# Optimization experiments

Measured on AMD Instinct MI355X. Metric: run time of the kernel, lower is better.

Reference implementation:

```python
import jax, jax.numpy as jnp
import numpy as np
from jax import lax

BIG = jnp.float32(1e6)  # sentinel 1D distance for rows with no edge pixel


def _maxpool3(x):
    # torch MaxPool2d(kernel_size=3, stride=1, padding=1) on NCHW; pad value -inf
    return lax.reduce_window(x, -jnp.inf, lax.max,
                             window_dimensions=(1, 1, 3, 3),
                             window_strides=(1, 1, 1, 1),
                             padding='SAME')


def _gen_edge(bool_map):
    # eroded = bool_map AND bool(maxpool((~bool_map).float()))
    pooled = _maxpool3(jnp.logical_not(bool_map).astype(jnp.float32))
    return jnp.logical_and(bool_map, pooled > 0).astype(jnp.int32)


def _dist1d(edge):
    # 1D distance along last axis (W) to nearest edge==1 pixel. edge: [B,1,H,W] int
    e = jnp.moveaxis(edge, -1, 0)  # [W,B,1,H]
    init = jnp.full(e.shape[1:], BIG, dtype=jnp.float32)

    def step(carry, ei):
        d = jnp.where(ei > 0, jnp.float32(0.0), carry + 1.0)
        return d, d

    _, dfwd = lax.scan(step, init, e)
    _, dbwd = lax.scan(step, init, e[::-1])
    g = jnp.minimum(dfwd, dbwd[::-1])          # [W,B,1,H]
    return jnp.minimum(jnp.moveaxis(g, 0, -1), BIG)  # [B,1,H,W]


def _edt(edge):
    # Exact Euclidean distance transform to nearest edge==1 pixel (separable,
    # Felzenszwalb-Huttenlocher formulation: d^2(y,x) = min_y' (y-y')^2 + g(y',x)^2).
    g = _dist1d(edge)          # [B,1,H,W]
    g2 = (g * g)[:, 0]         # [B,H,W]
    H = edge.shape[2]
    y = jnp.arange(H, dtype=jnp.float32)
    ydiff2 = (y[:, None] - y[None, :]) ** 2   # [H, H'] squared row offsets

    def per_img(g2img):  # g2img: [H,W] -> [H,W]
        return jnp.min(ydiff2[:, :, None] + g2img[None, :, :], axis=1)

    d2 = lax.map(per_img, g2)  # sequential over batch to bound the [H,H,W] temp
    return jnp.sqrt(d2)[:, None]  # [B,1,H,W]


def setup_inputs() -> dict:
    key = jax.random.key(0)
    kp, kt = jax.random.split(key)
    B, C, H, W = 16, 1, 256, 256
    pred = jax.random.uniform(kp, (B, C, H, W), dtype=jnp.float32)
    target = jax.random.uniform(kt, (B, C, H, W), dtype=jnp.float32)
    return {"pred": pred, "target": target}


def reference(pred, target):
    pred_b = pred > 0.5
    target_b = target > 0.5
    pred_edge = _gen_edge(pred_b)      # [B,1,H,W] int32 in {0,1}
    target_edge = _gen_edge(target_b)  # [B,1,H,W] int32 in {0,1}
    # scipy: distance_transform_edt(1-edge) * (1-edge) => dist to nearest edge, 0 on edge
    target_dist = _edt(target_edge) * (1 - target_edge).astype(jnp.float32)
    multiplied = pred_edge.astype(jnp.float32) * target_dist
    return jnp.mean(multiplied)
```

## Files before the change

kernel.cpp:

```cpp
#include <hip/hip_runtime.h>
#include <math.h>

#define H 256
#define W 256
#define BATCH 16
#define XT 16

__device__ __constant__ float kBIG = 1.0e6f;

__global__ __launch_bounds__(256) void k_rowdist(const float* __restrict__ target,
                                                 float* __restrict__ g2out) {
    const int y = blockIdx.x;
    const int b = blockIdx.y;
    const int x = threadIdx.x;
    const float* timg = target + (size_t)b * H * W;

    __shared__ int   nt[3][W + 2];
    __shared__ float A[W], Bv[W];

    if (x < 3) { nt[x][0] = 0; nt[x][W + 1] = 0; }
    nt[0][x + 1] = (y > 0)     ? ((timg[(y - 1) * W + x] > 0.5f) ? 0 : 1) : 0;
    nt[1][x + 1] =               ((timg[ y      * W + x] > 0.5f) ? 0 : 1);
    nt[2][x + 1] = (y < H - 1) ? ((timg[(y + 1) * W + x] > 0.5f) ? 0 : 1) : 0;
    __syncthreads();

    int holes = 0;
    #pragma unroll
    for (int r = 0; r < 3; ++r)
        holes |= nt[r][x] | nt[r][x + 1] | nt[r][x + 2];
    const int edge = (nt[1][x + 1] == 0) && holes;

    const float f = edge ? 0.0f : 1.0e6f;
    A[x]  = f - (float)x;
    Bv[x] = f + (float)x;
    __syncthreads();

    #pragma unroll
    for (int off = 1; off < W; off <<= 1) {
        float va = (x >= off)    ? A[x - off]   : 3.0e38f;
        float vb = (x + off < W) ? Bv[x + off]  : 3.0e38f;
        __syncthreads();
        A[x]  = fminf(A[x],  va);
        Bv[x] = fminf(Bv[x], vb);
        __syncthreads();
    }

    float g = fminf((float)x + A[x], Bv[x] - (float)x);
    g = fminf(g, 1.0e6f);
    g2out[((size_t)b * H + y) * W + x] = g * g;
}

__global__ __launch_bounds__(256) void k_edt(const float* __restrict__ g2,
                                             const float* __restrict__ pred,
                                             float* __restrict__ out) {
    const int b  = blockIdx.y;
    const int x0 = blockIdx.x * XT;
    const int t  = threadIdx.x;

    __shared__ float         g2s[H][XT];
    __shared__ unsigned char ph[H + 2][XT + 2];
    __shared__ float         red[256];

    const float* gimg = g2   + (size_t)b * H * W;
    const float* pimg = pred + (size_t)b * H * W;

    #pragma unroll
    for (int i = 0; i < (H * XT) / 256; ++i) {
        int idx = t + i * 256;
        int yy = idx / XT, xx = idx % XT;
        g2s[yy][xx] = gimg[yy * W + x0 + xx];
    }
    for (int idx = t; idx < (H + 2) * (XT + 2); idx += 256) {
        int yy = idx / (XT + 2);
        int xx = idx % (XT + 2);
        int gy = yy - 1, gx = x0 + xx - 1;
        unsigned char v = 0;
        if (gy >= 0 && gy < H && gx >= 0 && gx < W)
            v = (pimg[gy * W + gx] > 0.5f) ? 0 : 1;
        ph[yy][xx] = v;
    }
    __syncthreads();

    const int xl = t & (XT - 1);
    const int yb = t >> 4;
    float yv[16], m[16];
    #pragma unroll
    for (int j = 0; j < 16; ++j) { yv[j] = (float)(yb + 16 * j); m[j] = 3.0e38f; }

    for (int yp = 0; yp < H; ++yp) {
        float gv  = g2s[yp][xl];
        float fyp = (float)yp;
        #pragma unroll
        for (int j = 0; j < 16; ++j) {
            float dy = yv[j] - fyp;
            m[j] = fminf(m[j], fmaf(dy, dy, gv));
        }
    }

    float local = 0.0f;
    #pragma unroll
    for (int j = 0; j < 16; ++j) {
        int y = yb + 16 * j;
        int holes = 0;
        #pragma unroll
        for (int r = 0; r < 3; ++r)
            holes |= ph[y + r][xl] | ph[y + r][xl + 1] | ph[y + r][xl + 2];
        int edge = (ph[y + 1][xl + 1] == 0) && holes;
        if (edge) local += sqrtf(m[j]);
    }

    red[t] = local;
    __syncthreads();
    #pragma unroll
    for (int s = 128; s > 0; s >>= 1) {
        if (t < s) red[t] += red[t + s];
        __syncthreads();
    }
    if (t == 0)
        atomicAdd(out, red[0] * (1.0f / ((float)BATCH * H * W)));
}

extern "C" void kernel_launch(void* const* d_in, const int* in_sizes, int n_in,
                              void* d_out, int out_size, void* d_ws, size_t ws_size,
                              hipStream_t stream) {
    const float* pred   = (const float*)d_in[0];
    const float* target = (const float*)d_in[1];
    float* out = (float*)d_out;
    float* g2  = (float*)d_ws;

    hipMemsetAsync(d_out, 0, sizeof(float), stream);

    dim3 grid1(H, BATCH);
    k_rowdist<<<grid1, 256, 0, stream>>>(target, g2);

    dim3 grid2(W / XT, BATCH);
    k_edt<<<grid2, 256, 0, stream>>>(g2, pred, out);
}
```

Before: 103.0 us.

## Use wavefront shuffles for scans and reductions and split EDT over row tiles

Replaces the shared-memory Hillis-Steele min-scan in the row-distance kernel with wavefront shuffle scans plus a per-wave total combine. The EDT kernel gets a third grid dimension over 64-row tiles, so there are four times as many blocks, each with fewer accumulators per thread. Its block reduction becomes a shuffle reduction. The output memset is folded into the first kernel, saving a separate launch. The trade-off is that each EDT block reloads the full g2 column strip, so global traffic for g2 rises fourfold.

```diff
diff --git a/kernel.cpp b/kernel.cpp
--- a/kernel.cpp
+++ b/kernel.cpp
@@ -5,18 +5,21 @@
 #define W 256
 #define BATCH 16
 #define XT 16
-
-__device__ __constant__ float kBIG = 1.0e6f;
+#define YT 64
 
 __global__ __launch_bounds__(256) void k_rowdist(const float* __restrict__ target,
-                                                 float* __restrict__ g2out) {
+                                                 float* __restrict__ g2out,
+                                                 float* __restrict__ out) {
     const int y = blockIdx.x;
     const int b = blockIdx.y;
     const int x = threadIdx.x;
+
+    if (b == 0 && y == 0 && x == 0) out[0] = 0.0f;
+
     const float* timg = target + (size_t)b * H * W;
 
     __shared__ int   nt[3][W + 2];
-    __shared__ float A[W], Bv[W];
+    __shared__ float wtotA[4], wtotB[4];
 
     if (x < 3) { nt[x][0] = 0; nt[x][W + 1] = 0; }
     nt[0][x + 1] = (y > 0)     ? ((timg[(y - 1) * W + x] > 0.5f) ? 0 : 1) : 0;
@@ -31,21 +34,29 @@
     const int edge = (nt[1][x + 1] == 0) && holes;
 
     const float f = edge ? 0.0f : 1.0e6f;
-    A[x]  = f - (float)x;
-    Bv[x] = f + (float)x;
-    __syncthreads();
+    float A  = f - (float)x;
+    float Bv = f + (float)x;
+
+    const int lane = x & 63;
+    const int wv   = x >> 6;
 
     #pragma unroll
-    for (int off = 1; off < W; off <<= 1) {
-        float va = (x >= off)    ? A[x - off]   : 3.0e38f;
-        float vb = (x + off < W) ? Bv[x + off]  : 3.0e38f;
-        __syncthreads();
-        A[x]  = fminf(A[x],  va);
-        Bv[x] = fminf(Bv[x], vb);
-        __syncthreads();
+    for (int off = 1; off < 64; off <<= 1) {
+        float va = __shfl_up(A, off, 64);
+        if (lane >= off) A = fminf(A, va);
+        float vb = __shfl_down(Bv, off, 64);
+        if (lane < 64 - off) Bv = fminf(Bv, vb);
+    }
+    if (lane == 63) wtotA[wv] = A;
+    if (lane == 0)  wtotB[wv] = Bv;
+    __syncthreads();
+    #pragma unroll
+    for (int w2 = 0; w2 < 4; ++w2) {
+        if (w2 < wv) A  = fminf(A,  wtotA[w2]);
+        if (w2 > wv) Bv = fminf(Bv, wtotB[w2]);
     }
 
-    float g = fminf((float)x + A[x], Bv[x] - (float)x);
+    float g = fminf((float)x + A, Bv - (float)x);
     g = fminf(g, 1.0e6f);
     g2out[((size_t)b * H + y) * W + x] = g * g;
 }
@@ -53,13 +64,14 @@
 __global__ __launch_bounds__(256) void k_edt(const float* __restrict__ g2,
                                              const float* __restrict__ pred,
                                              float* __restrict__ out) {
-    const int b  = blockIdx.y;
+    const int b  = blockIdx.z;
+    const int y0 = blockIdx.y * YT;
     const int x0 = blockIdx.x * XT;
     const int t  = threadIdx.x;
 
     __shared__ float         g2s[H][XT];
-    __shared__ unsigned char ph[H + 2][XT + 2];
-    __shared__ float         red[256];
+    __shared__ unsigned char ph[YT + 2][XT + 2];
+    __shared__ float         red[4];
 
     const float* gimg = g2   + (size_t)b * H * W;
     const float* pimg = pred + (size_t)b * H * W;
@@ -67,13 +79,13 @@
     #pragma unroll
     for (int i = 0; i < (H * XT) / 256; ++i) {
         int idx = t + i * 256;
-        int yy = idx / XT, xx = idx % XT;
+        int yy = idx >> 4, xx = idx & 15;
         g2s[yy][xx] = gimg[yy * W + x0 + xx];
     }
-    for (int idx = t; idx < (H + 2) * (XT + 2); idx += 256) {
+    for (int idx = t; idx < (YT + 2) * (XT + 2); idx += 256) {
         int yy = idx / (XT + 2);
         int xx = idx % (XT + 2);
-        int gy = yy - 1, gx = x0 + xx - 1;
+        int gy = y0 + yy - 1, gx = x0 + xx - 1;
         unsigned char v = 0;
         if (gy >= 0 && gy < H && gx >= 0 && gx < W)
             v = (pimg[gy * W + gx] > 0.5f) ? 0 : 1;
@@ -83,41 +95,46 @@
 
     const int xl = t & (XT - 1);
     const int yb = t >> 4;
-    float yv[16], m[16];
+    float yv[4], m[4];
     #pragma unroll
-    for (int j = 0; j < 16; ++j) { yv[j] = (float)(yb + 16 * j); m[j] = 3.0e38f; }
+    for (int j = 0; j < 4; ++j) {
+        yv[j] = (float)(y0 + yb + 16 * j);
+        m[j]  = 3.0e38f;
+    }
 
-    for (int yp = 0; yp < H; ++yp) {
-        float gv  = g2s[yp][xl];
-        float fyp = (float)yp;
+    for (int yp = 0; yp < H; yp += 4) {
         #pragma unroll
-        for (int j = 0; j < 16; ++j) {
-            float dy = yv[j] - fyp;
-            m[j] = fminf(m[j], fmaf(dy, dy, gv));
+        for (int u = 0; u < 4; ++u) {
+            float gv  = g2s[yp + u][xl];
+            float fyp = (float)(yp + u);
+            #pragma unroll
+            for (int j = 0; j < 4; ++j) {
+                float dy = yv[j] - fyp;
+                m[j] = fminf(m[j], fmaf(dy, dy, gv));
+            }
         }
     }
 
     float local = 0.0f;
     #pragma unroll
-    for (int j = 0; j < 16; ++j) {
-        int y = yb + 16 * j;
+    for (int j = 0; j < 4; ++j) {
+        int yy = yb + 16 * j;
         int holes = 0;
         #pragma unroll
         for (int r = 0; r < 3; ++r)
-            holes |= ph[y + r][xl] | ph[y + r][xl + 1] | ph[y + r][xl + 2];
-        int edge = (ph[y + 1][xl + 1] == 0) && holes;
+            holes |= ph[yy + r][xl] | ph[yy + r][xl + 1] | ph[yy + r][xl + 2];
+        int edge = (ph[yy + 1][xl + 1] == 0) && holes;
         if (edge) local += sqrtf(m[j]);
     }
 
-    red[t] = local;
+    #pragma unroll
+    for (int off = 32; off > 0; off >>= 1)
+        local += __shfl_down(local, off, 64);
+    if ((t & 63) == 0) red[t >> 6] = local;
     __syncthreads();
-    #pragma unroll
-    for (int s = 128; s > 0; s >>= 1) {
-        if (t < s) red[t] += red[t + s];
-        __syncthreads();
-    }
     if (t == 0)
-        atomicAdd(out, red[0] * (1.0f / ((float)BATCH * H * W)));
+        atomicAdd(out, (red[0] + red[1] + red[2] + red[3]) *
+                           (1.0f / ((float)BATCH * H * W)));
 }
 
 extern "C" void kernel_launch(void* const* d_in, const int* in_sizes, int n_in,
@@ -128,11 +145,9 @@
     float* out = (float*)d_out;
     float* g2  = (float*)d_ws;
 
-    hipMemsetAsync(d_out, 0, sizeof(float), stream);
+    dim3 grid1(H, BATCH);
+    k_rowdist<<<grid1, 256, 0, stream>>>(target, g2, out);
 
-    dim3 grid1(H, BATCH);
-    k_rowdist<<<grid1, 256, 0, stream>>>(target, g2);
-
-    dim3 grid2(W / XT, BATCH);
+    dim3 grid2(W / XT, H / YT, BATCH);
     k_edt<<<grid2, 256, 0, stream>>>(g2, pred, out);
 }
```

After: 89.82 us. 12.8% less time.
